# Kernel optimization log

Hardware: AMD Instinct MI355X
Metric: run time of the kernel (lower is better)

## Reference

```python
import jax, jax.numpy as jnp
import numpy as np

N_ROUTES = 7      # len(ROUTES): 3 unimodal + 3 bimodal + 1 trimodal routes
PC_DIM = 512      # primary capsule pose dim
MC_DIM = 128      # output (decision) capsule pose dim
K = 25            # num_classes (phenotypes)
NUM_ROUTING = 3   # routing iterations
B = 4096


def _layer_norm(x, gamma, beta, eps=1e-5):
    mu = jnp.mean(x, axis=-1, keepdims=True)
    var = jnp.var(x, axis=-1, keepdims=True)
    return (x - mu) * jax.lax.rsqrt(var + eps) * gamma + beta


def setup_inputs() -> dict:
    key = jax.random.key(0)
    ks = jax.random.split(key, 4)
    w_std = float(np.sqrt(K / (PC_DIM * N_ROUTES)))  # CapsuleFC weight init scale
    return {
        "prim_pose": jax.random.normal(ks[0], (B, N_ROUTES, PC_DIM), dtype=jnp.float32),
        "prim_act": jax.random.uniform(ks[1], (B, N_ROUTES), dtype=jnp.float32),
        "w": w_std * jax.random.normal(ks[2], (N_ROUTES, PC_DIM, K, MC_DIM), dtype=jnp.float32),
        "ln_gamma": jnp.ones((MC_DIM,), dtype=jnp.float32),
        "ln_beta": jnp.zeros((MC_DIM,), dtype=jnp.float32),
        "embedding": 0.02 * jax.random.normal(ks[3], (K, MC_DIM), dtype=jnp.float32),
        "bias": jnp.zeros((K,), dtype=jnp.float32),
    }


def reference(prim_pose, prim_act, w, ln_gamma, ln_beta, embedding, bias):
    # prim_pose: [B, N, D_in]; prim_act: [B, N]
    act = prim_act[..., None]                      # [B, N, 1]
    scale = 1.0 / np.sqrt(MC_DIM)
    # Votes are constant across routing iterations; hoist out of the loop.
    vote = jnp.einsum('bnd,ndmv->bnmv', prim_pose, w)  # [B, N, K, Dv]
    next_pose = None
    routing_coef = None
    for it in range(NUM_ROUTING):
        if next_pose is None:
            # iteration 0: uniform routing coefficients (softmax of zeros over out capsules)
            routing_coef = jnp.full((prim_pose.shape[0], N_ROUTES, K), 1.0 / K,
                                    dtype=prim_pose.dtype)
        else:
            # inverted dot-product attention: agreement between votes and current decision pose
            agree = jnp.einsum('bnmv,bmv->bnm', vote, next_pose) * scale
            routing_coef = jax.nn.softmax(agree, axis=-1)
        c = routing_coef * act                     # weight routing by primary activations
        next_pose = _layer_norm(jnp.einsum('bnm,bnmv->bmv', c, vote), ln_gamma, ln_beta)
        # act_type='ONES' -> decision activations are all ones (no effect on routing)
    logits = jnp.einsum('bmd,md->bm', next_pose, embedding) + bias  # [B, K]
    return logits, prim_act, routing_coef
```

## Files before the change

kernel.cpp:

```cpp
#include <hip/hip_runtime.h>
#include <hip/hip_bf16.h>
#include <math.h>

#define N_ROUTES 7
#define PC_DIM   512
#define MC_DIM   128
#define KCLS     25
#define BATCH    4096

#define ROW_IN   (N_ROUTES * PC_DIM)
#define JDIM     (KCLS * MC_DIM)
#define VOTE_B   (N_ROUTES * JDIM)

typedef __attribute__((ext_vector_type(8))) _Float16 half8;
typedef __attribute__((ext_vector_type(4))) float f32x4;

__device__ inline ushort f2h(float f) {
    _Float16 h = (_Float16)f;
    return __builtin_bit_cast(ushort, h);
}

__device__ inline float2 h2f2(uint u) {
    union { uint x; _Float16 h[2]; } c; c.x = u;
    return make_float2((float)c.h[0], (float)c.h[1]);
}

__device__ inline void load_lds16(const void* g, void* l) {
    __builtin_amdgcn_global_load_lds(
        (const __attribute__((address_space(1))) void*)g,
        (__attribute__((address_space(3))) void*)l, 16, 0, 0);
}

__global__ __launch_bounds__(256) void conv_pose(const float* __restrict__ p,
                                                 ushort* __restrict__ pb, int n8) {
    int i = blockIdx.x * 256 + threadIdx.x;
    if (i >= n8) return;
    const float4* s = (const float4*)p + (size_t)i * 2;
    float4 a = s[0], b = s[1];
    ushort t[8];
    t[0]=f2h(a.x); t[1]=f2h(a.y); t[2]=f2h(a.z); t[3]=f2h(a.w);
    t[4]=f2h(b.x); t[5]=f2h(b.y); t[6]=f2h(b.z); t[7]=f2h(b.w);
    *(uint4*)(pb + (size_t)i * 8) = *(uint4*)t;
}

__global__ __launch_bounds__(256) void conv_w(const float* __restrict__ w,
                                              ushort* __restrict__ wt) {
    __shared__ float t[32][33];
    const int j0 = blockIdx.x * 32, d0 = blockIdx.y * 32, r = blockIdx.z;
    const int c = threadIdx.x & 31, rr = threadIdx.x >> 5;
    const float* wp = w + (size_t)r * PC_DIM * JDIM;
#pragma unroll
    for (int i = 0; i < 4; i++)
        t[rr + i * 8][c] = wp[(size_t)(d0 + rr + i * 8) * JDIM + j0 + c];
    __syncthreads();
    ushort* op = wt + (size_t)r * JDIM * PC_DIM;
#pragma unroll
    for (int i = 0; i < 4; i++)
        op[(size_t)(j0 + rr + i * 8) * PC_DIM + d0 + c] = f2h(t[c][rr + i * 8]);
}

#define GBM 128
#define GBN 128
#define GBK 64

__global__ __launch_bounds__(256) void vote_gemm_mfma(
        const ushort* __restrict__ poseb,
        const ushort* __restrict__ wt,
        ushort* __restrict__ vote,
        int rows) {
    int route, rowTile, jTile;
    if (gridDim.x == 5600) {
        const int x = blockIdx.x & 7;
        const int g = blockIdx.x >> 3;
        const int q = g / 25;
        jTile = g - q * 25;
        const int p = x * 28 + q;
        route = p >> 5;
        rowTile = p & 31;
    } else {
        const int nrt = gridDim.x / (N_ROUTES * 25);
        route = blockIdx.x / (nrt * 25);
        const int r2 = blockIdx.x - route * nrt * 25;
        rowTile = r2 / 25;
        jTile = r2 - rowTile * 25;
    }
    const int b0 = rowTile * GBM;
    const int j0 = jTile * GBN;

    __shared__ __align__(16) char smem[32768];
    ushort* As = (ushort*)smem;
    ushort* Bs = As + GBM * GBK;

    const int tid = threadIdx.x;
    const int l = tid & 63, w = tid >> 6;
    const int wm = w >> 1, wn = w & 1;

    f32x4 acc[4][4] = {};

    const ushort* Aptr = poseb + (size_t)route * PC_DIM;
    const ushort* Bptr = wt + (size_t)route * JDIM * PC_DIM;

    const int q4 = l >> 4;
    const int swz = l & 7;

    for (int k0 = 0; k0 < PC_DIM; k0 += GBK) {
        int f = tid;
#pragma unroll
        for (int i = 0; i < 4; i++, f += 256) {
            const int row = f >> 3;
            const int c = f & 7;
            const int qg = c ^ (row & 7);
            int ga = b0 + row; if (ga >= rows) ga = rows - 1;
            load_lds16(Aptr + (size_t)ga * ROW_IN + k0 + qg * 8, As + (size_t)f * 8);
            load_lds16(Bptr + (size_t)(j0 + row) * PC_DIM + k0 + qg * 8, Bs + (size_t)f * 8);
        }
        __syncthreads();

#pragma unroll
        for (int s = 0; s < 2; s++) {
            half8 af[4], bfg[4];
#pragma unroll
            for (int t = 0; t < 4; t++) {
                const int rowA = wm * 64 + t * 16 + (l & 15);
                const int rowB = wn * 64 + t * 16 + (l & 15);
                const int c = (s * 4 + q4) ^ swz;
                af[t]  = *(const half8*)(As + (size_t)(rowA * 8 + c) * 8);
                bfg[t] = *(const half8*)(Bs + (size_t)(rowB * 8 + c) * 8);
            }
#pragma unroll
            for (int mt = 0; mt < 4; mt++)
#pragma unroll
                for (int nt = 0; nt < 4; nt++)
                    acc[mt][nt] = __builtin_amdgcn_mfma_f32_16x16x32_f16(
                        af[mt], bfg[nt], acc[mt][nt], 0, 0, 0);
        }
        __syncthreads();
    }

    float* ep = (float*)smem + w * 16 * 68;
    const int erow = l >> 2;
    const int ec0  = (l & 3) * 16;
#pragma unroll
    for (int mt = 0; mt < 4; mt++) {
#pragma unroll
        for (int nt = 0; nt < 4; nt++)
#pragma unroll
            for (int i = 0; i < 4; i++)
                ep[((l >> 4) * 4 + i) * 68 + nt * 16 + (l & 15)] = acc[mt][nt][i];
        __syncthreads();
        const int grow = b0 + wm * 64 + mt * 16 + erow;
        if (grow < rows) {
            ushort t16[16];
#pragma unroll
            for (int t8 = 0; t8 < 4; t8++) {
                float4 v = *(float4*)&ep[erow * 68 + ec0 + t8 * 4];
                t16[t8*4+0]=f2h(v.x); t16[t8*4+1]=f2h(v.y);
                t16[t8*4+2]=f2h(v.z); t16[t8*4+3]=f2h(v.w);
            }
            ushort* dst = vote + (size_t)grow * VOTE_B + route * JDIM + j0 + wn * 64 + ec0;
            ((uint4*)dst)[0] = ((uint4*)t16)[0];
            ((uint4*)dst)[1] = ((uint4*)t16)[1];
        }
        __syncthreads();
    }
}

__global__ __launch_bounds__(448) void routing_kernel(
        const ushort* __restrict__ vote16,
        const float* __restrict__ act,
        const float* __restrict__ gamma,
        const float* __restrict__ beta,
        const float* __restrict__ emb,
        const float* __restrict__ bias,
        float* __restrict__ out_logits,
        float* __restrict__ out_act,
        float* __restrict__ out_coef) {
    const int b = blockIdx.x;
    __shared__ float coef_s[N_ROUTES * KCLS];
    __shared__ float act_s[8];

    const int tid = threadIdx.x, l = tid & 63, wv = tid >> 6;
    const int sub = l & 15, mg = l >> 4;
    const int m = wv + 7 * mg;
    const bool mv = (m < KCLS);

    if (tid < N_ROUTES) {
        float a = act[(size_t)b * N_ROUTES + tid];
        act_s[tid] = a;
        out_act[(size_t)b * N_ROUTES + tid] = a;
    }

    float vf[N_ROUTES][8];
    if (mv) {
        const uint4* vb = (const uint4*)(vote16 + (size_t)b * VOTE_B);
#pragma unroll
        for (int n = 0; n < N_ROUTES; n++) {
            uint4 q = vb[n * 400 + m * 16 + sub];
            float2 f0 = h2f2(q.x), f1 = h2f2(q.y), f2 = h2f2(q.z), f3 = h2f2(q.w);
            vf[n][0] = f0.x; vf[n][1] = f0.y; vf[n][2] = f1.x; vf[n][3] = f1.y;
            vf[n][4] = f2.x; vf[n][5] = f2.y; vf[n][6] = f3.x; vf[n][7] = f3.y;
        }
    } else {
#pragma unroll
        for (int n = 0; n < N_ROUTES; n++)
#pragma unroll
            for (int j = 0; j < 8; j++) vf[n][j] = 0.f;
    }
    const int mc = mv ? m : 24;

    float g[8], be[8];
    *(float4*)(g)      = *(const float4*)(gamma + 8 * sub);
    *(float4*)(g + 4)  = *(const float4*)(gamma + 8 * sub + 4);
    *(float4*)(be)     = *(const float4*)(beta  + 8 * sub);
    *(float4*)(be + 4) = *(const float4*)(beta  + 8 * sub + 4);
    __syncthreads();

    const float scale = 0.088388347648318447f;
    float pose[8];

    auto update = [&](bool first) {
        float r[8];
#pragma unroll
        for (int j = 0; j < 8; j++) r[j] = 0.f;
#pragma unroll
        for (int n = 0; n < N_ROUTES; n++) {
            float c = first ? (act_s[n] * 0.04f) : (coef_s[n * KCLS + mc] * act_s[n]);
#pragma unroll
            for (int j = 0; j < 8; j++) r[j] += c * vf[n][j];
        }
        float S = 0.f, Q = 0.f;
#pragma unroll
        for (int j = 0; j < 8; j++) { S += r[j]; Q += r[j] * r[j]; }
#pragma unroll
        for (int o = 8; o; o >>= 1) {
            S += __shfl_xor(S, o);
            Q += __shfl_xor(Q, o);
        }
        float mean = S * 0.0078125f;
        float var  = Q * 0.0078125f - mean * mean;
        float rs   = rsqrtf(var + 1e-5f);
#pragma unroll
        for (int j = 0; j < 8; j++) pose[j] = (r[j] - mean) * rs * g[j] + be[j];
    };

    update(true);
    __syncthreads();

    const int sgrp = tid >> 5, slane = tid & 31;

    for (int it = 1; it < 3; it++) {
        float d[N_ROUTES];
#pragma unroll
        for (int n = 0; n < N_ROUTES; n++) {
            float t = 0.f;
#pragma unroll
            for (int j = 0; j < 8; j++) t += vf[n][j] * pose[j];
            d[n] = t;
        }
#pragma unroll
        for (int o = 8; o; o >>= 1)
#pragma unroll
            for (int n = 0; n < N_ROUTES; n++) d[n] += __shfl_xor(d[n], o);
        if (sub == 0 && mv) {
#pragma unroll
            for (int n = 0; n < N_ROUTES; n++) coef_s[n * KCLS + m] = d[n] * scale;
        }
        __syncthreads();
        if (sgrp < N_ROUTES) {
            float c = (slane < KCLS) ? coef_s[sgrp * KCLS + slane] : -1e30f;
            float mx = c;
#pragma unroll
            for (int o = 16; o; o >>= 1) mx = fmaxf(mx, __shfl_xor(mx, o, 32));
            float e = (slane < KCLS) ? expf(c - mx) : 0.f;
            float s = e;
#pragma unroll
            for (int o = 16; o; o >>= 1) s += __shfl_xor(s, o, 32);
            if (slane < KCLS) coef_s[sgrp * KCLS + slane] = e / s;
        }
        __syncthreads();
        update(false);
        if (it == 1) __syncthreads();
    }

    float e[8];
    *(float4*)(e)     = *(const float4*)(emb + mc * MC_DIM + 8 * sub);
    *(float4*)(e + 4) = *(const float4*)(emb + mc * MC_DIM + 8 * sub + 4);
    float dd = 0.f;
#pragma unroll
    for (int j = 0; j < 8; j++) dd += pose[j] * e[j];
#pragma unroll
    for (int o = 8; o; o >>= 1) dd += __shfl_xor(dd, o);
    if (sub == 0 && mv) out_logits[(size_t)b * KCLS + m] = dd + bias[m];

    if (tid < N_ROUTES * KCLS)
        out_coef[(size_t)b * (N_ROUTES * KCLS) + tid] = coef_s[tid];
}

extern "C" void kernel_launch(void* const* d_in, const int* in_sizes, int n_in,
                              void* d_out, int out_size, void* d_ws, size_t ws_size,
                              hipStream_t stream) {
    const float* pose  = (const float*)d_in[0];
    const float* act   = (const float*)d_in[1];
    const float* w     = (const float*)d_in[2];
    const float* gamma = (const float*)d_in[3];
    const float* beta  = (const float*)d_in[4];
    const float* emb   = (const float*)d_in[5];
    const float* bias  = (const float*)d_in[6];

    float* out        = (float*)d_out;
    float* out_logits = out;
    float* out_act    = out + BATCH * KCLS;
    float* out_coef   = out + BATCH * KCLS + BATCH * N_ROUTES;

    const size_t wt_bytes    = (size_t)N_ROUTES * JDIM * PC_DIM * 2;
    const size_t poseb_bytes = (size_t)BATCH * ROW_IN * 2;
    ushort* wt    = (ushort*)d_ws;
    ushort* poseb = (ushort*)((char*)d_ws + wt_bytes);
    ushort* voteh = (ushort*)((char*)d_ws + wt_bytes + poseb_bytes);

    size_t rem = ws_size > wt_bytes + poseb_bytes ? ws_size - wt_bytes - poseb_bytes : 0;
    size_t cap = rem / ((size_t)VOTE_B * 2);
    int chunk;
    if (cap >= (size_t)BATCH)  chunk = BATCH;
    else if (cap >= 128)       chunk = (int)(cap & ~(size_t)127);
    else                       chunk = (int)(cap > 0 ? cap : 1);

    conv_w<<<dim3(JDIM / 32, PC_DIM / 32, N_ROUTES), 256, 0, stream>>>(w, wt);
    const int n8 = BATCH * ROW_IN / 8;
    conv_pose<<<(n8 + 255) / 256, 256, 0, stream>>>(pose, poseb, n8);

    for (int b0 = 0; b0 < BATCH; b0 += chunk) {
        int rows = BATCH - b0 < chunk ? BATCH - b0 : chunk;
        int nRowTiles = (rows + GBM - 1) / GBM;
        vote_gemm_mfma<<<nRowTiles * N_ROUTES * 25, 256, 0, stream>>>(
            poseb + (size_t)b0 * ROW_IN, wt, voteh, rows);
        routing_kernel<<<rows, 448, 0, stream>>>(
            voteh,
            act + (size_t)b0 * N_ROUTES,
            gamma, beta, emb, bias,
            out_logits + (size_t)b0 * KCLS,
            out_act    + (size_t)b0 * N_ROUTES,
            out_coef   + (size_t)b0 * N_ROUTES * KCLS);
    }
}
```

Measured before the change: 344.7 us.

## Rewrite vote GEMM with 256x256 tiles and a 4-stage async LDS pipeline

Replaces the 128x128x64 single-buffered vote GEMM with 256x256 block tiles using 512 threads and a 4-deep ring of 32-wide K stages loaded asynchronously into LDS. Explicit vmcnt/lgkmcnt waits, sched barriers and s_setprio let MFMA work overlap with the next stage's global loads. The grid tile mapping changes to 13 j-tiles per route, with padded columns clamped on load and masked on store. This aims to raise arithmetic intensity and hide load latency, at the cost of 128 KB LDS per block, heavier register use, and about 4% wasted work on padded j-tiles.

```diff
diff --git a/kernel.cpp b/kernel.cpp
--- a/kernel.cpp
+++ b/kernel.cpp
@@ -59,97 +59,138 @@
         op[(size_t)(j0 + rr + i * 8) * PC_DIM + d0 + c] = f2h(t[c][rr + i * 8]);
 }
 
-#define GBM 128
-#define GBN 128
-#define GBK 64
-
-__global__ __launch_bounds__(256) void vote_gemm_mfma(
+
+#define BAR() do { __builtin_amdgcn_sched_barrier(0); \
+                   __builtin_amdgcn_s_barrier(); \
+                   __builtin_amdgcn_sched_barrier(0); } while (0)
+#define WAIT_LGKM0() do { asm volatile("s_waitcnt lgkmcnt(0)" ::: "memory"); \
+                          __builtin_amdgcn_sched_barrier(0); } while (0)
+#define WAIT_VM(n) do { asm volatile("s_waitcnt vmcnt(" #n ")" ::: "memory"); } while (0)
+
+__global__ __launch_bounds__(512, 2) void vote_gemm_mfma(
         const ushort* __restrict__ poseb,
         const ushort* __restrict__ wt,
         ushort* __restrict__ vote,
         int rows) {
+    __shared__ __align__(16) char smem[131072];
+
     int route, rowTile, jTile;
-    if (gridDim.x == 5600) {
+    if (gridDim.x == 1456) {
         const int x = blockIdx.x & 7;
         const int g = blockIdx.x >> 3;
-        const int q = g / 25;
-        jTile = g - q * 25;
-        const int p = x * 28 + q;
-        route = p >> 5;
-        rowTile = p & 31;
+        const int q = g / 91;
+        const int rem = g - q * 91;
+        route = rem / 13;
+        jTile = rem - route * 13;
+        rowTile = x * 2 + q;
     } else {
-        const int nrt = gridDim.x / (N_ROUTES * 25);
-        route = blockIdx.x / (nrt * 25);
-        const int r2 = blockIdx.x - route * nrt * 25;
-        rowTile = r2 / 25;
-        jTile = r2 - rowTile * 25;
-    }
-    const int b0 = rowTile * GBM;
-    const int j0 = jTile * GBN;
-
-    __shared__ __align__(16) char smem[32768];
-    ushort* As = (ushort*)smem;
-    ushort* Bs = As + GBM * GBK;
+        rowTile = blockIdx.x / 91;
+        const int rem = blockIdx.x - rowTile * 91;
+        route = rem / 13;
+        jTile = rem - route * 13;
+    }
+    const int b0 = rowTile * 256;
+    const int j0 = jTile * 256;
 
     const int tid = threadIdx.x;
     const int l = tid & 63, w = tid >> 6;
-    const int wm = w >> 1, wn = w & 1;
-
-    f32x4 acc[4][4] = {};
+    const int wm = w >> 2, wn = w & 3;
+    const int lm = l & 15, q4 = l >> 4;
+    const int xr = (l >> 1) & 3;
 
     const ushort* Aptr = poseb + (size_t)route * PC_DIM;
     const ushort* Bptr = wt + (size_t)route * JDIM * PC_DIM;
 
-    const int q4 = l >> 4;
-    const int swz = l & 7;
-
-    for (int k0 = 0; k0 < PC_DIM; k0 += GBK) {
-        int f = tid;
-#pragma unroll
-        for (int i = 0; i < 4; i++, f += 256) {
-            const int row = f >> 3;
-            const int c = f & 7;
-            const int qg = c ^ (row & 7);
-            int ga = b0 + row; if (ga >= rows) ga = rows - 1;
-            load_lds16(Aptr + (size_t)ga * ROW_IN + k0 + qg * 8, As + (size_t)f * 8);
-            load_lds16(Bptr + (size_t)(j0 + row) * PC_DIM + k0 + qg * 8, Bs + (size_t)f * 8);
-        }
-        __syncthreads();
-
-#pragma unroll
-        for (int s = 0; s < 2; s++) {
-            half8 af[4], bfg[4];
-#pragma unroll
-            for (int t = 0; t < 4; t++) {
-                const int rowA = wm * 64 + t * 16 + (l & 15);
-                const int rowB = wn * 64 + t * 16 + (l & 15);
-                const int c = (s * 4 + q4) ^ swz;
-                af[t]  = *(const half8*)(As + (size_t)(rowA * 8 + c) * 8);
-                bfg[t] = *(const half8*)(Bs + (size_t)(rowB * 8 + c) * 8);
-            }
-#pragma unroll
-            for (int mt = 0; mt < 4; mt++)
-#pragma unroll
-                for (int nt = 0; nt < 4; nt++)
-                    acc[mt][nt] = __builtin_amdgcn_mfma_f32_16x16x32_f16(
-                        af[mt], bfg[nt], acc[mt][nt], 0, 0, 0);
-        }
-        __syncthreads();
-    }
-
-    float* ep = (float*)smem + w * 16 * 68;
-    const int erow = l >> 2;
-    const int ec0  = (l & 3) * 16;
-#pragma unroll
-    for (int mt = 0; mt < 4; mt++) {
+    uint aof0, aof1, bof0, bof1;
+    {
+        int f, row, c, qg, ga, jr;
+        f = tid;        row = f >> 2; c = f & 3; qg = c ^ ((row >> 1) & 3);
+        ga = b0 + row; if (ga >= rows) ga = rows - 1;
+        aof0 = (uint)ga * ROW_IN + qg * 8;
+        jr = j0 + row; if (jr >= JDIM) jr = JDIM - 1;
+        bof0 = (uint)jr * PC_DIM + qg * 8;
+        f = tid + 512;  row = f >> 2; c = f & 3; qg = c ^ ((row >> 1) & 3);
+        ga = b0 + row; if (ga >= rows) ga = rows - 1;
+        aof1 = (uint)ga * ROW_IN + qg * 8;
+        jr = j0 + row; if (jr >= JDIM) jr = JDIM - 1;
+        bof1 = (uint)jr * PC_DIM + qg * 8;
+    }
+
+    const int aBase = ((wm * 128 + lm) * 4 + (q4 ^ xr)) * 16;
+    const int bBase = 16384 + ((wn * 64 + lm) * 4 + (q4 ^ xr)) * 16;
+
+    f32x4 acc[8][4] = {};
+
+#define STAGE_A(kt) do { \
+        char* d_ = smem + (((kt) & 3) * 32768); \
+        load_lds16(Aptr + aof0 + (kt) * 32, d_ + (size_t)tid * 16); \
+        load_lds16(Aptr + aof1 + (kt) * 32, d_ + (size_t)(tid + 512) * 16); \
+    } while (0)
+#define STAGE_B(kt) do { \
+        char* d_ = smem + (((kt) & 3) * 32768) + 16384; \
+        load_lds16(Bptr + bof0 + (kt) * 32, d_ + (size_t)tid * 16); \
+        load_lds16(Bptr + bof1 + (kt) * 32, d_ + (size_t)(tid + 512) * 16); \
+    } while (0)
+
+    STAGE_A(0); STAGE_B(0);
+    STAGE_A(1); STAGE_B(1);
+    STAGE_A(2); STAGE_B(2);
+    WAIT_VM(8);
+    BAR();
+
+    half8 af[4], bf[4];
+
+#define TILE(t, SA, SB, VM) do { \
+        const char* bp_ = smem + (((t) & 3) * 32768); \
+        _Pragma("unroll") for (int nt = 0; nt < 4; nt++) \
+            bf[nt] = *(const half8*)(bp_ + bBase + nt * 1024); \
+        _Pragma("unroll") for (int mt = 0; mt < 4; mt++) \
+            af[mt] = *(const half8*)(bp_ + aBase + mt * 1024); \
+        SA; \
+        BAR(); \
+        WAIT_LGKM0(); \
+        __builtin_amdgcn_s_setprio(1); \
+        _Pragma("unroll") for (int mt = 0; mt < 4; mt++) \
+        _Pragma("unroll") for (int nt = 0; nt < 4; nt++) \
+            acc[mt][nt] = __builtin_amdgcn_mfma_f32_16x16x32_f16( \
+                af[mt], bf[nt], acc[mt][nt], 0, 0, 0); \
+        __builtin_amdgcn_s_setprio(0); \
+        BAR(); \
+        _Pragma("unroll") for (int mt = 0; mt < 4; mt++) \
+            af[mt] = *(const half8*)(bp_ + aBase + (mt + 4) * 1024); \
+        SB; \
+        BAR(); \
+        WAIT_LGKM0(); \
+        __builtin_amdgcn_s_setprio(1); \
+        _Pragma("unroll") for (int mt = 0; mt < 4; mt++) \
+        _Pragma("unroll") for (int nt = 0; nt < 4; nt++) \
+            acc[mt + 4][nt] = __builtin_amdgcn_mfma_f32_16x16x32_f16( \
+                af[mt], bf[nt], acc[mt + 4][nt], 0, 0, 0); \
+        __builtin_amdgcn_s_setprio(0); \
+        VM; \
+        BAR(); \
+    } while (0)
+
+    for (int t = 0; t < 13; ++t)
+        TILE(t, STAGE_A(t + 3), STAGE_B(t + 3), WAIT_VM(8));
+    TILE(13, , , WAIT_VM(4));
+    TILE(14, , , WAIT_VM(0));
+    TILE(15, , , );
+
+    float* ep = (float*)smem + w * 1088;
+    const int erow = l >> 2, ec0 = (l & 3) * 16;
+    const int jv = j0 + wn * 64;
+    const bool jok = jv < JDIM;
+#pragma unroll
+    for (int mt = 0; mt < 8; mt++) {
 #pragma unroll
         for (int nt = 0; nt < 4; nt++)
 #pragma unroll
             for (int i = 0; i < 4; i++)
-                ep[((l >> 4) * 4 + i) * 68 + nt * 16 + (l & 15)] = acc[mt][nt][i];
-        __syncthreads();
-        const int grow = b0 + wm * 64 + mt * 16 + erow;
-        if (grow < rows) {
+                ep[(q4 * 4 + i) * 68 + nt * 16 + lm] = acc[mt][nt][i];
+        asm volatile("s_waitcnt lgkmcnt(0)" ::: "memory");
+        const int grow = b0 + wm * 128 + mt * 16 + erow;
+        if (jok && grow < rows) {
             ushort t16[16];
 #pragma unroll
             for (int t8 = 0; t8 < 4; t8++) {
@@ -157,11 +198,11 @@
                 t16[t8*4+0]=f2h(v.x); t16[t8*4+1]=f2h(v.y);
                 t16[t8*4+2]=f2h(v.z); t16[t8*4+3]=f2h(v.w);
             }
-            ushort* dst = vote + (size_t)grow * VOTE_B + route * JDIM + j0 + wn * 64 + ec0;
+            ushort* dst = vote + (size_t)grow * VOTE_B + route * JDIM + jv + ec0;
             ((uint4*)dst)[0] = ((uint4*)t16)[0];
             ((uint4*)dst)[1] = ((uint4*)t16)[1];
         }
-        __syncthreads();
+        asm volatile("s_waitcnt lgkmcnt(0)" ::: "memory");
     }
 }
 
@@ -331,8 +372,8 @@
 
     for (int b0 = 0; b0 < BATCH; b0 += chunk) {
         int rows = BATCH - b0 < chunk ? BATCH - b0 : chunk;
-        int nRowTiles = (rows + GBM - 1) / GBM;
-        vote_gemm_mfma<<<nRowTiles * N_ROUTES * 25, 256, 0, stream>>>(
+        int nRowTiles = (rows + 255) / 256;
+        vote_gemm_mfma<<<nRowTiles * N_ROUTES * 13, 512, 0, stream>>>(
             poseb + (size_t)b0 * ROW_IN, wt, voteh, rows);
         routing_kernel<<<rows, 448, 0, stream>>>(
             voteh,
```

Measured after the change: 347.3 us. Within noise of the previous version (+0.7%).

## Triple-buffer vote GEMM with async LDS loads and cap batch chunk

Applied to the files above, without the earlier changes.

Rewrites the vote GEMM main loop as a three-stage LDS pipeline with K-step 32, prefetching two tiles ahead with explicit vmcnt waits and one barrier per step. It adds MFMA priority raising, occupancy hints, a new block-to-tile mapping that groups the 8 XCDs by row tiles, and drops the epilogue barriers in favour of per-wave LDS waits. It also caps the batch chunk at 2048 so the fp16 vote buffer stays smaller and is more likely to stay in cache between GEMM and routing, at the cost of an extra pair of launches.

```diff
diff --git a/kernel.cpp b/kernel.cpp
--- a/kernel.cpp
+++ b/kernel.cpp
@@ -59,95 +59,119 @@
         op[(size_t)(j0 + rr + i * 8) * PC_DIM + d0 + c] = f2h(t[c][rr + i * 8]);
 }
 
-#define GBM 128
-#define GBN 128
-#define GBK 64
-
-__global__ __launch_bounds__(256) void vote_gemm_mfma(
+
+#define BAR() do { __builtin_amdgcn_sched_barrier(0); \
+                   __builtin_amdgcn_s_barrier(); \
+                   __builtin_amdgcn_sched_barrier(0); } while (0)
+#define WAIT_LGKM0() do { asm volatile("s_waitcnt lgkmcnt(0)" ::: "memory"); \
+                          __builtin_amdgcn_sched_barrier(0); } while (0)
+#define WAIT_VM(n) do { asm volatile("s_waitcnt vmcnt(" #n ")" ::: "memory"); } while (0)
+
+__global__ __launch_bounds__(256, 3) void vote_gemm_mfma(
         const ushort* __restrict__ poseb,
         const ushort* __restrict__ wt,
         ushort* __restrict__ vote,
         int rows) {
+    __shared__ __align__(16) char smem[49152];
+
     int route, rowTile, jTile;
-    if (gridDim.x == 5600) {
-        const int x = blockIdx.x & 7;
-        const int g = blockIdx.x >> 3;
-        const int q = g / 25;
-        jTile = g - q * 25;
-        const int p = x * 28 + q;
-        route = p >> 5;
-        rowTile = p & 31;
-    } else {
-        const int nrt = gridDim.x / (N_ROUTES * 25);
-        route = blockIdx.x / (nrt * 25);
-        const int r2 = blockIdx.x - route * nrt * 25;
-        rowTile = r2 / 25;
-        jTile = r2 - rowTile * 25;
-    }
-    const int b0 = rowTile * GBM;
-    const int j0 = jTile * GBN;
-
-    __shared__ __align__(16) char smem[32768];
-    ushort* As = (ushort*)smem;
-    ushort* Bs = As + GBM * GBK;
+    {
+        const int blk = blockIdx.x;
+        const int nrt = gridDim.x / 175;
+        if ((nrt & 7) == 0) {
+            const int per = nrt >> 3;
+            const int x = blk & 7;
+            const int g = blk >> 3;
+            const int q = g / 175;
+            const int rem = g - q * 175;
+            route = rem / 25;
+            jTile = rem - route * 25;
+            rowTile = x * per + q;
+        } else {
+            rowTile = blk / 175;
+            const int rem = blk - rowTile * 175;
+            route = rem / 25;
+            jTile = rem - route * 25;
+        }
+    }
+    const int b0 = rowTile * 128;
+    const int j0 = jTile * 128;
 
     const int tid = threadIdx.x;
     const int l = tid & 63, w = tid >> 6;
     const int wm = w >> 1, wn = w & 1;
-
-    f32x4 acc[4][4] = {};
+    const int lm = l & 15, q4 = l >> 4;
+    const int xr = (l >> 1) & 3;
 
     const ushort* Aptr = poseb + (size_t)route * PC_DIM;
     const ushort* Bptr = wt + (size_t)route * JDIM * PC_DIM;
 
-    const int q4 = l >> 4;
-    const int swz = l & 7;
-
-    for (int k0 = 0; k0 < PC_DIM; k0 += GBK) {
-        int f = tid;
-#pragma unroll
-        for (int i = 0; i < 4; i++, f += 256) {
-            const int row = f >> 3;
-            const int c = f & 7;
-            const int qg = c ^ (row & 7);
-            int ga = b0 + row; if (ga >= rows) ga = rows - 1;
-            load_lds16(Aptr + (size_t)ga * ROW_IN + k0 + qg * 8, As + (size_t)f * 8);
-            load_lds16(Bptr + (size_t)(j0 + row) * PC_DIM + k0 + qg * 8, Bs + (size_t)f * 8);
-        }
-        __syncthreads();
-
-#pragma unroll
-        for (int s = 0; s < 2; s++) {
-            half8 af[4], bfg[4];
-#pragma unroll
-            for (int t = 0; t < 4; t++) {
-                const int rowA = wm * 64 + t * 16 + (l & 15);
-                const int rowB = wn * 64 + t * 16 + (l & 15);
-                const int c = (s * 4 + q4) ^ swz;
-                af[t]  = *(const half8*)(As + (size_t)(rowA * 8 + c) * 8);
-                bfg[t] = *(const half8*)(Bs + (size_t)(rowB * 8 + c) * 8);
-            }
-#pragma unroll
-            for (int mt = 0; mt < 4; mt++)
-#pragma unroll
-                for (int nt = 0; nt < 4; nt++)
-                    acc[mt][nt] = __builtin_amdgcn_mfma_f32_16x16x32_f16(
-                        af[mt], bfg[nt], acc[mt][nt], 0, 0, 0);
-        }
-        __syncthreads();
-    }
-
-    float* ep = (float*)smem + w * 16 * 68;
-    const int erow = l >> 2;
-    const int ec0  = (l & 3) * 16;
+    uint aof0, aof1, bof0, bof1;
+    {
+        int f, row, c, qg, ga;
+        f = tid;        row = f >> 2; c = f & 3; qg = c ^ ((row >> 1) & 3);
+        ga = b0 + row; if (ga >= rows) ga = rows - 1;
+        aof0 = (uint)ga * ROW_IN + qg * 8;
+        bof0 = (uint)(j0 + row) * PC_DIM + qg * 8;
+        f = tid + 256;  row = f >> 2; c = f & 3; qg = c ^ ((row >> 1) & 3);
+        ga = b0 + row; if (ga >= rows) ga = rows - 1;
+        aof1 = (uint)ga * ROW_IN + qg * 8;
+        bof1 = (uint)(j0 + row) * PC_DIM + qg * 8;
+    }
+
+    const int aBase = ((wm * 64 + lm) * 4 + (q4 ^ xr)) * 16;
+    const int bBase = 8192 + ((wn * 64 + lm) * 4 + (q4 ^ xr)) * 16;
+
+    f32x4 acc[4][4] = {};
+
+#define STAGE(kt) do { \
+        char* d_ = smem + (((kt) % 3) * 16384); \
+        load_lds16(Aptr + aof0 + (kt) * 32, d_ + (size_t)tid * 16); \
+        load_lds16(Aptr + aof1 + (kt) * 32, d_ + (size_t)(tid + 256) * 16); \
+        load_lds16(Bptr + bof0 + (kt) * 32, d_ + 8192 + (size_t)tid * 16); \
+        load_lds16(Bptr + bof1 + (kt) * 32, d_ + 8192 + (size_t)(tid + 256) * 16); \
+    } while (0)
+
+    STAGE(0); STAGE(1);
+    WAIT_VM(4);
+    BAR();
+
+    half8 af[4], bf[4];
+
+#pragma unroll
+    for (int t = 0; t < 16; ++t) {
+        if (t < 14) STAGE(t + 2);
+        const char* bp_ = smem + ((t % 3) * 16384);
+#pragma unroll
+        for (int nt = 0; nt < 4; nt++)
+            bf[nt] = *(const half8*)(bp_ + bBase + nt * 1024);
+#pragma unroll
+        for (int mt = 0; mt < 4; mt++)
+            af[mt] = *(const half8*)(bp_ + aBase + mt * 1024);
+        WAIT_LGKM0();
+        __builtin_amdgcn_s_setprio(1);
+#pragma unroll
+        for (int mt = 0; mt < 4; mt++)
+#pragma unroll
+            for (int nt = 0; nt < 4; nt++)
+                acc[mt][nt] = __builtin_amdgcn_mfma_f32_16x16x32_f16(
+                    af[mt], bf[nt], acc[mt][nt], 0, 0, 0);
+        __builtin_amdgcn_s_setprio(0);
+        if (t < 14)       WAIT_VM(4);
+        else if (t == 14) WAIT_VM(0);
+        BAR();
+    }
+
+    float* ep = (float*)smem + w * 1088;
+    const int erow = l >> 2, ec0 = (l & 3) * 16;
 #pragma unroll
     for (int mt = 0; mt < 4; mt++) {
 #pragma unroll
         for (int nt = 0; nt < 4; nt++)
 #pragma unroll
             for (int i = 0; i < 4; i++)
-                ep[((l >> 4) * 4 + i) * 68 + nt * 16 + (l & 15)] = acc[mt][nt][i];
-        __syncthreads();
+                ep[(q4 * 4 + i) * 68 + nt * 16 + lm] = acc[mt][nt][i];
+        asm volatile("s_waitcnt lgkmcnt(0)" ::: "memory");
         const int grow = b0 + wm * 64 + mt * 16 + erow;
         if (grow < rows) {
             ushort t16[16];
@@ -161,7 +185,7 @@
             ((uint4*)dst)[0] = ((uint4*)t16)[0];
             ((uint4*)dst)[1] = ((uint4*)t16)[1];
         }
-        __syncthreads();
+        asm volatile("s_waitcnt lgkmcnt(0)" ::: "memory");
     }
 }
 
@@ -321,9 +345,9 @@
     size_t rem = ws_size > wt_bytes + poseb_bytes ? ws_size - wt_bytes - poseb_bytes : 0;
     size_t cap = rem / ((size_t)VOTE_B * 2);
     int chunk;
-    if (cap >= (size_t)BATCH)  chunk = BATCH;
-    else if (cap >= 128)       chunk = (int)(cap & ~(size_t)127);
-    else                       chunk = (int)(cap > 0 ? cap : 1);
+    if (cap >= 2048)      chunk = 2048;
+    else if (cap >= 128)  chunk = (int)(cap & ~(size_t)127);
+    else                  chunk = (int)(cap > 0 ? cap : 1);
 
     conv_w<<<dim3(JDIM / 32, PC_DIM / 32, N_ROUTES), 256, 0, stream>>>(w, wt);
     const int n8 = BATCH * ROW_IN / 8;
@@ -331,8 +355,8 @@
 
     for (int b0 = 0; b0 < BATCH; b0 += chunk) {
         int rows = BATCH - b0 < chunk ? BATCH - b0 : chunk;
-        int nRowTiles = (rows + GBM - 1) / GBM;
-        vote_gemm_mfma<<<nRowTiles * N_ROUTES * 25, 256, 0, stream>>>(
+        int nRowTiles = (rows + 127) / 128;
+        vote_gemm_mfma<<<nRowTiles * 175, 256, 0, stream>>>(
             poseb + (size_t)b0 * ROW_IN, wt, voteh, rows);
         routing_kernel<<<rows, 448, 0, stream>>>(
             voteh,
```

New measurement: 355.0 us. +3.0%, slower.
